# Performance work log

Hardware: AMD Instinct MI355X
Metric: run time of the kernel (lower is better)

The kernel has to match this reference:

```python
import jax, jax.numpy as jnp
import numpy as np
from jax import lax


def _lstm_encode(x_seq, W_ih, W_hh, b_ih, b_hh):
    """Run a single-layer LSTM over x_seq (B,S,F); return final (h, c), each (B,H).
    PyTorch gate order: i, f, g, o."""
    B = x_seq.shape[0]
    H = W_hh.shape[1]
    # Precompute input projections for the whole sequence: (B,S,4H)
    xg = jnp.einsum('bsf,gf->bsg', x_seq, W_ih) + b_ih + b_hh

    def step(carry, xg_t):
        h, c = carry
        gates = xg_t + h @ W_hh.T  # (B,4H)
        i, f, g, o = jnp.split(gates, 4, axis=-1)
        c = jax.nn.sigmoid(f) * c + jax.nn.sigmoid(i) * jnp.tanh(g)
        h = jax.nn.sigmoid(o) * jnp.tanh(c)
        return (h, c), None

    h0 = jnp.zeros((B, H), dtype=x_seq.dtype)
    c0 = jnp.zeros((B, H), dtype=x_seq.dtype)
    (h, c), _ = lax.scan(step, (h0, c0), jnp.swapaxes(xg, 0, 1))
    return h, c


def setup_inputs() -> dict:
    key = jax.random.key(0)
    ks = jax.random.split(key, 8)
    B, S, F, H, T = 256, 512, 64, 1024, 64
    s_in = 1.0 / np.sqrt(F)
    s_h = 1.0 / np.sqrt(H)
    return {
        'input_sequence': jax.random.normal(ks[0], (B, S, F), dtype=jnp.float32),
        'W_ih_enc': jax.random.normal(ks[1], (4 * H, F), dtype=jnp.float32) * s_in,
        'W_hh_enc': jax.random.normal(ks[2], (4 * H, H), dtype=jnp.float32) * s_h,
        'b_ih_enc': jnp.zeros((4 * H,), dtype=jnp.float32),
        'b_hh_enc': jnp.zeros((4 * H,), dtype=jnp.float32),
        'W_ih_dec': jax.random.normal(ks[3], (4 * H, F), dtype=jnp.float32) * s_in,
        'W_hh_dec': jax.random.normal(ks[4], (4 * H, H), dtype=jnp.float32) * s_h,
        'b_ih_dec': jnp.zeros((4 * H,), dtype=jnp.float32),
        'b_hh_dec': jnp.zeros((4 * H,), dtype=jnp.float32),
        'W_fc': jax.random.normal(ks[5], (F, H), dtype=jnp.float32) * s_h,
        'b_fc': jnp.zeros((F,), dtype=jnp.float32),
        'prediction_length': T,
    }


def reference(input_sequence, W_ih_enc, W_hh_enc, b_ih_enc, b_hh_enc,
              W_ih_dec, W_hh_dec, b_ih_dec, b_hh_dec, W_fc, b_fc,
              prediction_length):
    # Encoder: summarize past sequence into final (h, c)
    h, c = _lstm_encode(input_sequence, W_ih_enc, W_hh_enc, b_ih_enc, b_hh_enc)

    b_dec = b_ih_dec + b_hh_dec
    x0 = input_sequence[:, -1, :]  # (B,F) last observed step

    def dec_step(carry, _):
        h, c, x = carry
        gates = x @ W_ih_dec.T + h @ W_hh_dec.T + b_dec  # (B,4H)
        i, f, g, o = jnp.split(gates, 4, axis=-1)
        c = jax.nn.sigmoid(f) * c + jax.nn.sigmoid(i) * jnp.tanh(g)
        h = jax.nn.sigmoid(o) * jnp.tanh(c)
        pred = h @ W_fc.T + b_fc  # (B,F)
        return (h, c, pred), pred

    _, preds = lax.scan(dec_step, (h, c, x0), None, length=prediction_length)
    # preds: (T,B,F) -> (B,T,F)
    return jnp.swapaxes(preds, 0, 1)
```

## Files before the change

kernel.cpp:

```cpp
#include <hip/hip_runtime.h>
#include <hip/hip_cooperative_groups.h>
#include <stdint.h>
#include <stddef.h>

namespace cg = cooperative_groups;


typedef short s16x8 __attribute__((ext_vector_type(8)));
typedef short s16x4 __attribute__((ext_vector_type(4)));
typedef float f32x4 __attribute__((ext_vector_type(4)));
typedef float f32x16 __attribute__((ext_vector_type(16)));

#define LDS_BYTES  156416
#define RED_OFF    139264
#define BIASG_OFF  155904
#define BIASFC_OFF 156160

#define WS_FLAGS 0
#define WS_HRING 12288
#define WS_WFC   4206592

#define HBUF_ELEMS 262144
#define GO_BASE    2304

__device__ __forceinline__ unsigned short f2bf(float f) {
  union { unsigned int i; float f; } v;
  v.f = f;
  unsigned int i = v.i;
  return (unsigned short)((i + 0x7FFFu + ((i >> 16) & 1u)) >> 16);
}
__device__ __forceinline__ float sigm(float x) { return 1.f / (1.f + __expf(-x)); }
__device__ __forceinline__ float tanh_f(float x) {
  float e = __expf(2.f * x);
  return 1.f - 2.f / (e + 1.f);
}

__device__ __forceinline__ void load_wg(unsigned short* wl, float* biasg,
    const float* Wih, const float* Whh, const float* bih, const float* bhh,
    int n, int wave, int lane, int tid) {
  const int l31 = lane & 31;
  const int kh8 = (lane >> 5) << 3;
  for (int f = wave; f < 136; f += 4) {
    const int s  = f >> 1;
    const int t2 = f & 1;
    const int col = t2 * 32 + l31;
    const int k0  = s * 16 + kh8;
    const int r   = (col >> 4) * 1024 + n * 16 + (col & 15);
    const float* src = (s < 4) ? (Wih + (size_t)r * 64 + k0)
                               : (Whh + (size_t)r * 1024 + (k0 - 64));
    s16x8 w;
#pragma unroll
    for (int j = 0; j < 8; ++j) ((unsigned short*)&w)[j] = f2bf(src[j]);
    *(s16x8*)(wl + (size_t)f * 512 + lane * 8) = w;
  }
  if (tid < 64) {
    const int r = (tid >> 4) * 1024 + n * 16 + (tid & 15);
    biasg[tid] = bih[r] + bhh[r];
  }
}

__device__ __forceinline__ void red_write(float* red, const f32x16 (&acc)[2][2],
                                          int lane, const float* bias) {
#pragma unroll
  for (int mi = 0; mi < 2; ++mi)
#pragma unroll
    for (int t2 = 0; t2 < 2; ++t2)
#pragma unroll
      for (int r = 0; r < 16; ++r) {
        const int row = mi * 32 + (r & 3) + ((r >> 2) << 3) + ((lane >> 5) << 2);
        const int col = t2 * 32 + (lane & 31);
        float v = acc[mi][t2][r];
        if (bias) v += bias[col];
        red[row * 65 + col] = v;
      }
}
__device__ __forceinline__ void red_add(float* red, const f32x16 (&acc)[2][2],
                                        int lane) {
#pragma unroll
  for (int mi = 0; mi < 2; ++mi)
#pragma unroll
    for (int t2 = 0; t2 < 2; ++t2)
#pragma unroll
      for (int r = 0; r < 16; ++r) {
        const int row = mi * 32 + (r & 3) + ((r >> 2) << 3) + ((lane >> 5) << 2);
        const int col = t2 * 32 + (lane & 31);
        atomicAdd(red + row * 65 + col, acc[mi][t2][r]);
      }
}

__global__ void __launch_bounds__(256, 1) seq2seq_lstm(
    const float* __restrict__ xin,
    const float* __restrict__ Wih_e,
    const float* __restrict__ Whh_e,
    const float* __restrict__ bih_e,
    const float* __restrict__ bhh_e,
    const float* __restrict__ Wih_d,
    const float* __restrict__ Whh_d,
    const float* __restrict__ bih_d,
    const float* __restrict__ bhh_d,
    const float* __restrict__ Wfc,
    const float* __restrict__ bfc,
    float* __restrict__ out,
    unsigned short* __restrict__ hring,
    unsigned short* __restrict__ wfcb,
    unsigned int* __restrict__ flags) {
  extern __shared__ char smem[];
  unsigned short* wl = (unsigned short*)smem;
  float* red    = (float*)(smem + RED_OFF);
  float* biasg  = (float*)(smem + BIASG_OFF);
  float* biasfc = (float*)(smem + BIASFC_OFF);

  cg::grid_group grid = cg::this_grid();

  const int tid  = threadIdx.x;
  const int wave = tid >> 6;
  const int lane = tid & 63;
  const int wg   = blockIdx.x;
  const int m    = wg & 3;
  const int n    = wg >> 2;
  const int bm   = m << 6;
  const int l31  = lane & 31;
  const int kh8  = (lane >> 5) << 3;
  const int ks0  = wave * 17;
  const int ab   = tid >> 2;
  const int au0  = (tid & 3) << 2;

  load_wg(wl, biasg, Wih_e, Whh_e, bih_e, bhh_e, n, wave, lane, tid);

  {
    unsigned short* hinit = hring + (size_t)7 * HBUF_ELEMS;
    const size_t hq = ((size_t)(bm + ab) * 1024 + n * 16 + au0) >> 2;
    __hip_atomic_store((unsigned long long*)hinit + hq, 0ull,
                       __ATOMIC_RELAXED, __HIP_MEMORY_SCOPE_AGENT);
    const int wi = wg * 256 + tid;
    wfcb[wi] = f2bf(Wfc[wi]);
    if (tid < 9)
      __hip_atomic_store(flags + wg * 9 + tid, 0u,
                         __ATOMIC_RELAXED, __HIP_MEMORY_SCOPE_AGENT);
    if (wg == 0 && tid < 16)
      __hip_atomic_store(flags + GO_BASE + tid * 32, 0u,
                         __ATOMIC_RELAXED, __HIP_MEMORY_SCOPE_AGENT);
  }
  __syncthreads();
  grid.sync();

  float cst[4] = {0.f, 0.f, 0.f, 0.f};

  for (int gs = 0; gs < 576; ++gs) {
    const bool dec = (gs >= 512);
    const int t = gs - 512;

    if ((gs & 7) == 0 && gs != 0) {
      if (tid == 0) __builtin_amdgcn_fence(__ATOMIC_ACQUIRE, "agent");
      __syncthreads();
    }

    if (gs == 512) {
      __syncthreads();
      load_wg(wl, biasg, Wih_d, Whh_d, bih_d, bhh_d, n, wave, lane, tid);
      if (tid < 64) biasfc[tid] = bfc[tid];
      __syncthreads();
    }
    const unsigned short* hb = hring + (size_t)((gs + 7) & 7) * HBUF_ELEMS;
    unsigned short* hnx      = hring + (size_t)(gs & 7) * HBUF_ELEMS;

    s16x8 areg[17][2];
#pragma unroll
    for (int i = 0; i < 17; ++i) {
      const int s = ks0 + i;
      if (s < 4) {
        const int fk = s * 16 + kh8;
        if (!dec || t == 0) {
          const int tt = dec ? 511 : gs;
          const float* p = xin + (size_t)(bm + l31) * 32768 + tt * 64 + fk;
#pragma unroll
          for (int mi = 0; mi < 2; ++mi) {
            const float* pp = p + (size_t)mi * 32 * 32768;
            s16x8 av;
#pragma unroll
            for (int j = 0; j < 8; ++j) ((unsigned short*)&av)[j] = f2bf(pp[j]);
            areg[i][mi] = av;
          }
        } else {
#pragma unroll
          for (int mi = 0; mi < 2; ++mi) {
            s16x8 av;
#pragma unroll
            for (int j = 0; j < 8; ++j)
              ((unsigned short*)&av)[j] = f2bf(red[(mi * 32 + l31) * 65 + fk + j]);
            areg[i][mi] = av;
          }
        }
      } else {
        const int k = (s - 4) * 16 + kh8;
        const unsigned short* p = hb + (size_t)(bm + l31) * 1024 + k;
        areg[i][0] = *(const s16x8*)p;
        areg[i][1] = *(const s16x8*)(p + 32 * 1024);
      }
    }

    f32x16 acc[2][2] = {};
#pragma unroll
    for (int i = 0; i < 17; ++i) {
      const int s = ks0 + i;
      const s16x8 b0 = *(const s16x8*)(wl + (size_t)(s * 2 + 0) * 512 + lane * 8);
      const s16x8 b1 = *(const s16x8*)(wl + (size_t)(s * 2 + 1) * 512 + lane * 8);
      acc[0][0] = __builtin_amdgcn_mfma_f32_32x32x16_bf16(areg[i][0], b0, acc[0][0], 0, 0, 0);
      acc[1][0] = __builtin_amdgcn_mfma_f32_32x32x16_bf16(areg[i][1], b0, acc[1][0], 0, 0, 0);
      acc[0][1] = __builtin_amdgcn_mfma_f32_32x32x16_bf16(areg[i][0], b1, acc[0][1], 0, 0, 0);
      acc[1][1] = __builtin_amdgcn_mfma_f32_32x32x16_bf16(areg[i][1], b1, acc[1][1], 0, 0, 0);
    }

    if (wave == 0) red_write(red, acc, lane, nullptr);
    __syncthreads();
    if (wave != 0) red_add(red, acc, lane);
    __syncthreads();

    {
      float hn[4];
#pragma unroll
      for (int j = 0; j < 4; ++j) {
        const int u = au0 + j;
        const float gi = red[ab * 65 + u]      + biasg[u];
        const float gf = red[ab * 65 + 16 + u] + biasg[16 + u];
        const float gg = red[ab * 65 + 32 + u] + biasg[32 + u];
        const float go = red[ab * 65 + 48 + u] + biasg[48 + u];
        const float c = sigm(gf) * cst[j] + sigm(gi) * tanh_f(gg);
        cst[j] = c;
        hn[j] = sigm(go) * tanh_f(c);
      }
      union { unsigned short u[4]; unsigned long long ull; } pk;
#pragma unroll
      for (int j = 0; j < 4; ++j) pk.u[j] = f2bf(hn[j]);
      const size_t hq = ((size_t)(bm + ab) * 1024 + n * 16 + au0) >> 2;
      __hip_atomic_store((unsigned long long*)hnx + hq, pk.ull,
                         __ATOMIC_RELAXED, __HIP_MEMORY_SCOPE_AGENT);
    }
    __syncthreads();

    if (tid == 0) {
      unsigned int* fl = flags + m * 576 + gs;
      unsigned int old = __hip_atomic_fetch_add(fl, 1u, __ATOMIC_RELAXED,
                                                __HIP_MEMORY_SCOPE_AGENT);
      if (old == 63u) {
        const unsigned int stamp = (unsigned int)gs + 1u;
#pragma unroll
        for (int sb = 0; sb < 4; ++sb)
          __hip_atomic_store(flags + GO_BASE + (m * 4 + sb) * 32, stamp,
                             __ATOMIC_RELAXED, __HIP_MEMORY_SCOPE_AGENT);
      } else {
        unsigned int* go = flags + GO_BASE + (m * 4 + (n >> 4)) * 32;
        for (;;) {
          __builtin_amdgcn_s_sleep(8);
          unsigned int v = __hip_atomic_fetch_add(go, 0u, __ATOMIC_RELAXED,
                                                  __HIP_MEMORY_SCOPE_AGENT);
          if (v > (unsigned int)gs) break;
        }
      }
      if (dec) __builtin_amdgcn_fence(__ATOMIC_ACQUIRE, "agent");
    }
    __syncthreads();

    if (dec && (n == 0 || t < 63)) {
      f32x16 pacc[2][2] = {};
      const int ps0 = wave * 16;
#pragma unroll 4
      for (int i = 0; i < 16; ++i) {
        const int k = (ps0 + i) * 16 + kh8;
        const unsigned short* hp = hnx + (size_t)(bm + l31) * 1024 + k;
        const unsigned short* wp = wfcb + (size_t)l31 * 1024 + k;
        const s16x8 a0 = *(const s16x8*)hp;
        const s16x8 a1 = *(const s16x8*)(hp + 32 * 1024);
        const s16x8 b0 = *(const s16x8*)wp;
        const s16x8 b1 = *(const s16x8*)(wp + 32 * 1024);
        pacc[0][0] = __builtin_amdgcn_mfma_f32_32x32x16_bf16(a0, b0, pacc[0][0], 0, 0, 0);
        pacc[1][0] = __builtin_amdgcn_mfma_f32_32x32x16_bf16(a1, b0, pacc[1][0], 0, 0, 0);
        pacc[0][1] = __builtin_amdgcn_mfma_f32_32x32x16_bf16(a0, b1, pacc[0][1], 0, 0, 0);
        pacc[1][1] = __builtin_amdgcn_mfma_f32_32x32x16_bf16(a1, b1, pacc[1][1], 0, 0, 0);
      }
      if (wave == 0) red_write(red, pacc, lane, biasfc);
      __syncthreads();
      if (wave != 0) red_add(red, pacc, lane);
      __syncthreads();
      if (n == 0) {
        const int oc = (tid & 3) << 4;
        float* op = out + (size_t)(bm + ab) * 4096 + t * 64 + oc;
#pragma unroll
        for (int jj = 0; jj < 16; jj += 4) {
          f32x4 v = { red[ab * 65 + oc + jj],     red[ab * 65 + oc + jj + 1],
                      red[ab * 65 + oc + jj + 2], red[ab * 65 + oc + jj + 3] };
          *(f32x4*)(op + jj) = v;
        }
      }
      __syncthreads();
    }
  }
}

extern "C" void kernel_launch(void* const* d_in, const int* in_sizes, int n_in,
                              void* d_out, int out_size, void* d_ws, size_t ws_size,
                              hipStream_t stream) {
  (void)in_sizes; (void)n_in; (void)out_size; (void)ws_size;
  const float* xin   = (const float*)d_in[0];
  const float* Wih_e = (const float*)d_in[1];
  const float* Whh_e = (const float*)d_in[2];
  const float* bih_e = (const float*)d_in[3];
  const float* bhh_e = (const float*)d_in[4];
  const float* Wih_d = (const float*)d_in[5];
  const float* Whh_d = (const float*)d_in[6];
  const float* bih_d = (const float*)d_in[7];
  const float* bhh_d = (const float*)d_in[8];
  const float* Wfc   = (const float*)d_in[9];
  const float* bfc   = (const float*)d_in[10];
  float* out = (float*)d_out;

  char* ws = (char*)d_ws;
  unsigned int* flags   = (unsigned int*)(ws + WS_FLAGS);
  unsigned short* hring = (unsigned short*)(ws + WS_HRING);
  unsigned short* wfcb  = (unsigned short*)(ws + WS_WFC);

  hipFuncSetAttribute((const void*)seq2seq_lstm,
                      hipFuncAttributeMaxDynamicSharedMemorySize, LDS_BYTES);

  void* args[] = {
    (void*)&xin, (void*)&Wih_e, (void*)&Whh_e, (void*)&bih_e, (void*)&bhh_e,
    (void*)&Wih_d, (void*)&Whh_d, (void*)&bih_d, (void*)&bhh_d,
    (void*)&Wfc, (void*)&bfc, (void*)&out, (void*)&hring,
    (void*)&wfcb, (void*)&flags
  };
  hipLaunchCooperativeKernel((const void*)seq2seq_lstm, dim3(256), dim3(256),
                             args, LDS_BYTES, stream);
}
```

Measured before the change: 15.88 ms.

## Double workgroup to 512 threads, split M across waves, retile h ring layout

Workgroups grow from 4 to 8 waves, with each wave pair splitting the 64 batch rows into two 32-row halves, so each wave runs half the MFMAs per step and the per-step recurrent matmul critical path shrinks. The hidden-state ring buffer moves from row-major (batch, 1024) to k-slab-major (64 slabs of 16 columns, batch rows contiguous), so each wave's A-fragment loads and each workgroup's h stores are contiguous. Gate nonlinearities are spread over 512 threads with two units each. The cost is more waves contending for LDS atomics during the reduction and more per-step barrier overhead.

```diff
diff --git a/kernel.cpp b/kernel.cpp
--- a/kernel.cpp
+++ b/kernel.cpp
@@ -7,7 +7,6 @@
 
 
 typedef short s16x8 __attribute__((ext_vector_type(8)));
-typedef short s16x4 __attribute__((ext_vector_type(4)));
 typedef float f32x4 __attribute__((ext_vector_type(4)));
 typedef float f32x16 __attribute__((ext_vector_type(16)));
 
@@ -40,7 +39,7 @@
     int n, int wave, int lane, int tid) {
   const int l31 = lane & 31;
   const int kh8 = (lane >> 5) << 3;
-  for (int f = wave; f < 136; f += 4) {
+  for (int f = wave; f < 136; f += 8) {
     const int s  = f >> 1;
     const int t2 = f & 1;
     const int col = t2 * 32 + l31;
@@ -59,36 +58,32 @@
   }
 }
 
-__device__ __forceinline__ void red_write(float* red, const f32x16 (&acc)[2][2],
-                                          int lane, const float* bias) {
-#pragma unroll
-  for (int mi = 0; mi < 2; ++mi)
-#pragma unroll
-    for (int t2 = 0; t2 < 2; ++t2)
-#pragma unroll
-      for (int r = 0; r < 16; ++r) {
-        const int row = mi * 32 + (r & 3) + ((r >> 2) << 3) + ((lane >> 5) << 2);
-        const int col = t2 * 32 + (lane & 31);
-        float v = acc[mi][t2][r];
-        if (bias) v += bias[col];
-        red[row * 65 + col] = v;
-      }
-}
-__device__ __forceinline__ void red_add(float* red, const f32x16 (&acc)[2][2],
-                                        int lane) {
-#pragma unroll
-  for (int mi = 0; mi < 2; ++mi)
-#pragma unroll
-    for (int t2 = 0; t2 < 2; ++t2)
-#pragma unroll
-      for (int r = 0; r < 16; ++r) {
-        const int row = mi * 32 + (r & 3) + ((r >> 2) << 3) + ((lane >> 5) << 2);
-        const int col = t2 * 32 + (lane & 31);
-        atomicAdd(red + row * 65 + col, acc[mi][t2][r]);
-      }
-}
-
-__global__ void __launch_bounds__(256, 1) seq2seq_lstm(
+__device__ __forceinline__ void red_write32(float* red, const f32x16 (&acc)[2],
+                                            int lane, int mh, const float* bias) {
+#pragma unroll
+  for (int t2 = 0; t2 < 2; ++t2)
+#pragma unroll
+    for (int r = 0; r < 16; ++r) {
+      const int row = mh * 32 + (r & 3) + ((r >> 2) << 3) + ((lane >> 5) << 2);
+      const int col = t2 * 32 + (lane & 31);
+      float v = acc[t2][r];
+      if (bias) v += bias[col];
+      red[row * 65 + col] = v;
+    }
+}
+__device__ __forceinline__ void red_add32(float* red, const f32x16 (&acc)[2],
+                                          int lane, int mh) {
+#pragma unroll
+  for (int t2 = 0; t2 < 2; ++t2)
+#pragma unroll
+    for (int r = 0; r < 16; ++r) {
+      const int row = mh * 32 + (r & 3) + ((r >> 2) << 3) + ((lane >> 5) << 2);
+      const int col = t2 * 32 + (lane & 31);
+      atomicAdd(red + row * 65 + col, acc[t2][r]);
+    }
+}
+
+__global__ void __launch_bounds__(512, 1) seq2seq_lstm(
     const float* __restrict__ xin,
     const float* __restrict__ Wih_e,
     const float* __restrict__ Whh_e,
@@ -121,19 +116,21 @@
   const int bm   = m << 6;
   const int l31  = lane & 31;
   const int kh8  = (lane >> 5) << 3;
-  const int ks0  = wave * 17;
-  const int ab   = tid >> 2;
-  const int au0  = (tid & 3) << 2;
+  const int mh   = wave & 1;
+  const int q    = wave >> 1;
+  const int ks0  = q * 17;
+  const int mrow = bm + mh * 32 + l31;
+  const int ab   = tid >> 3;
+  const int au0  = (tid & 7) << 1;
 
   load_wg(wl, biasg, Wih_e, Whh_e, bih_e, bhh_e, n, wave, lane, tid);
 
   {
     unsigned short* hinit = hring + (size_t)7 * HBUF_ELEMS;
-    const size_t hq = ((size_t)(bm + ab) * 1024 + n * 16 + au0) >> 2;
-    __hip_atomic_store((unsigned long long*)hinit + hq, 0ull,
+    const size_t hq = ((size_t)n * 4096 + (size_t)(bm + ab) * 16 + au0) >> 1;
+    __hip_atomic_store((unsigned int*)hinit + hq, 0u,
                        __ATOMIC_RELAXED, __HIP_MEMORY_SCOPE_AGENT);
-    const int wi = wg * 256 + tid;
-    wfcb[wi] = f2bf(Wfc[wi]);
+    if (tid < 256) wfcb[wg * 256 + tid] = f2bf(Wfc[wg * 256 + tid]);
     if (tid < 9)
       __hip_atomic_store(flags + wg * 9 + tid, 0u,
                          __ATOMIC_RELAXED, __HIP_MEMORY_SCOPE_AGENT);
@@ -144,7 +141,7 @@
   __syncthreads();
   grid.sync();
 
-  float cst[4] = {0.f, 0.f, 0.f, 0.f};
+  float cst[2] = {0.f, 0.f};
 
   for (int gs = 0; gs < 576; ++gs) {
     const bool dec = (gs >= 512);
@@ -164,7 +161,7 @@
     const unsigned short* hb = hring + (size_t)((gs + 7) & 7) * HBUF_ELEMS;
     unsigned short* hnx      = hring + (size_t)(gs & 7) * HBUF_ELEMS;
 
-    s16x8 areg[17][2];
+    s16x8 areg[17];
 #pragma unroll
     for (int i = 0; i < 17; ++i) {
       const int s = ks0 + i;
@@ -172,54 +169,43 @@
         const int fk = s * 16 + kh8;
         if (!dec || t == 0) {
           const int tt = dec ? 511 : gs;
-          const float* p = xin + (size_t)(bm + l31) * 32768 + tt * 64 + fk;
-#pragma unroll
-          for (int mi = 0; mi < 2; ++mi) {
-            const float* pp = p + (size_t)mi * 32 * 32768;
-            s16x8 av;
-#pragma unroll
-            for (int j = 0; j < 8; ++j) ((unsigned short*)&av)[j] = f2bf(pp[j]);
-            areg[i][mi] = av;
-          }
+          const float* p = xin + (size_t)mrow * 32768 + tt * 64 + fk;
+          s16x8 av;
+#pragma unroll
+          for (int j = 0; j < 8; ++j) ((unsigned short*)&av)[j] = f2bf(p[j]);
+          areg[i] = av;
         } else {
-#pragma unroll
-          for (int mi = 0; mi < 2; ++mi) {
-            s16x8 av;
-#pragma unroll
-            for (int j = 0; j < 8; ++j)
-              ((unsigned short*)&av)[j] = f2bf(red[(mi * 32 + l31) * 65 + fk + j]);
-            areg[i][mi] = av;
-          }
+          s16x8 av;
+#pragma unroll
+          for (int j = 0; j < 8; ++j)
+            ((unsigned short*)&av)[j] = f2bf(red[(mh * 32 + l31) * 65 + fk + j]);
+          areg[i] = av;
         }
       } else {
-        const int k = (s - 4) * 16 + kh8;
-        const unsigned short* p = hb + (size_t)(bm + l31) * 1024 + k;
-        areg[i][0] = *(const s16x8*)p;
-        areg[i][1] = *(const s16x8*)(p + 32 * 1024);
-      }
-    }
-
-    f32x16 acc[2][2] = {};
+        areg[i] = *(const s16x8*)(hb + (size_t)(s - 4) * 4096 +
+                                  (size_t)mrow * 16 + kh8);
+      }
+    }
+
+    f32x16 acc[2] = {};
 #pragma unroll
     for (int i = 0; i < 17; ++i) {
       const int s = ks0 + i;
       const s16x8 b0 = *(const s16x8*)(wl + (size_t)(s * 2 + 0) * 512 + lane * 8);
       const s16x8 b1 = *(const s16x8*)(wl + (size_t)(s * 2 + 1) * 512 + lane * 8);
-      acc[0][0] = __builtin_amdgcn_mfma_f32_32x32x16_bf16(areg[i][0], b0, acc[0][0], 0, 0, 0);
-      acc[1][0] = __builtin_amdgcn_mfma_f32_32x32x16_bf16(areg[i][1], b0, acc[1][0], 0, 0, 0);
-      acc[0][1] = __builtin_amdgcn_mfma_f32_32x32x16_bf16(areg[i][0], b1, acc[0][1], 0, 0, 0);
-      acc[1][1] = __builtin_amdgcn_mfma_f32_32x32x16_bf16(areg[i][1], b1, acc[1][1], 0, 0, 0);
-    }
-
-    if (wave == 0) red_write(red, acc, lane, nullptr);
+      acc[0] = __builtin_amdgcn_mfma_f32_32x32x16_bf16(areg[i], b0, acc[0], 0, 0, 0);
+      acc[1] = __builtin_amdgcn_mfma_f32_32x32x16_bf16(areg[i], b1, acc[1], 0, 0, 0);
+    }
+
+    if (q == 0) red_write32(red, acc, lane, mh, nullptr);
     __syncthreads();
-    if (wave != 0) red_add(red, acc, lane);
+    if (q != 0) red_add32(red, acc, lane, mh);
     __syncthreads();
 
     {
-      float hn[4];
-#pragma unroll
-      for (int j = 0; j < 4; ++j) {
+      float hn[2];
+#pragma unroll
+      for (int j = 0; j < 2; ++j) {
         const int u = au0 + j;
         const float gi = red[ab * 65 + u]      + biasg[u];
         const float gf = red[ab * 65 + 16 + u] + biasg[16 + u];
@@ -229,11 +215,11 @@
         cst[j] = c;
         hn[j] = sigm(go) * tanh_f(c);
       }
-      union { unsigned short u[4]; unsigned long long ull; } pk;
-#pragma unroll
-      for (int j = 0; j < 4; ++j) pk.u[j] = f2bf(hn[j]);
-      const size_t hq = ((size_t)(bm + ab) * 1024 + n * 16 + au0) >> 2;
-      __hip_atomic_store((unsigned long long*)hnx + hq, pk.ull,
+      union { unsigned short u[2]; unsigned int ui; } pk;
+      pk.u[0] = f2bf(hn[0]);
+      pk.u[1] = f2bf(hn[1]);
+      const size_t hq = ((size_t)n * 4096 + (size_t)(bm + ab) * 16 + au0) >> 1;
+      __hip_atomic_store((unsigned int*)hnx + hq, pk.ui,
                          __ATOMIC_RELAXED, __HIP_MEMORY_SCOPE_AGENT);
     }
     __syncthreads();
@@ -262,31 +248,29 @@
     __syncthreads();
 
     if (dec && (n == 0 || t < 63)) {
-      f32x16 pacc[2][2] = {};
-      const int ps0 = wave * 16;
+      f32x16 pacc[2] = {};
+      const int ps0 = q * 16;
 #pragma unroll 4
       for (int i = 0; i < 16; ++i) {
         const int k = (ps0 + i) * 16 + kh8;
-        const unsigned short* hp = hnx + (size_t)(bm + l31) * 1024 + k;
+        const unsigned short* hp =
+            hnx + (size_t)(ps0 + i) * 4096 + (size_t)mrow * 16 + kh8;
         const unsigned short* wp = wfcb + (size_t)l31 * 1024 + k;
         const s16x8 a0 = *(const s16x8*)hp;
-        const s16x8 a1 = *(const s16x8*)(hp + 32 * 1024);
         const s16x8 b0 = *(const s16x8*)wp;
         const s16x8 b1 = *(const s16x8*)(wp + 32 * 1024);
-        pacc[0][0] = __builtin_amdgcn_mfma_f32_32x32x16_bf16(a0, b0, pacc[0][0], 0, 0, 0);
-        pacc[1][0] = __builtin_amdgcn_mfma_f32_32x32x16_bf16(a1, b0, pacc[1][0], 0, 0, 0);
-        pacc[0][1] = __builtin_amdgcn_mfma_f32_32x32x16_bf16(a0, b1, pacc[0][1], 0, 0, 0);
-        pacc[1][1] = __builtin_amdgcn_mfma_f32_32x32x16_bf16(a1, b1, pacc[1][1], 0, 0, 0);
-      }
-      if (wave == 0) red_write(red, pacc, lane, biasfc);
-      __syncthreads();
-      if (wave != 0) red_add(red, pacc, lane);
+        pacc[0] = __builtin_amdgcn_mfma_f32_32x32x16_bf16(a0, b0, pacc[0], 0, 0, 0);
+        pacc[1] = __builtin_amdgcn_mfma_f32_32x32x16_bf16(a0, b1, pacc[1], 0, 0, 0);
+      }
+      if (q == 0) red_write32(red, pacc, lane, mh, biasfc);
+      __syncthreads();
+      if (q != 0) red_add32(red, pacc, lane, mh);
       __syncthreads();
       if (n == 0) {
-        const int oc = (tid & 3) << 4;
+        const int oc = (tid & 7) << 3;
         float* op = out + (size_t)(bm + ab) * 4096 + t * 64 + oc;
 #pragma unroll
-        for (int jj = 0; jj < 16; jj += 4) {
+        for (int jj = 0; jj < 8; jj += 4) {
           f32x4 v = { red[ab * 65 + oc + jj],     red[ab * 65 + oc + jj + 1],
                       red[ab * 65 + oc + jj + 2], red[ab * 65 + oc + jj + 3] };
           *(f32x4*)(op + jj) = v;
@@ -328,6 +312,6 @@
     (void*)&Wfc, (void*)&bfc, (void*)&out, (void*)&hring,
     (void*)&wfcb, (void*)&flags
   };
-  hipLaunchCooperativeKernel((const void*)seq2seq_lstm, dim3(256), dim3(256),
+  hipLaunchCooperativeKernel((const void*)seq2seq_lstm, dim3(256), dim3(512),
                              args, LDS_BYTES, stream);
 }
```

Result: faster. 14.31 ms (-9.9%).
